# Kernel optimization log

Measured on AMD Instinct MI355X. Metric: run time of the kernel, lower is better.

Reference implementation:

```python
import jax, jax.numpy as jnp
import numpy as np

D_MODEL = 512
DK = 4
DV = 8
HIDD = 10
HEAD = D_MODEL // DV  # 64
LN_EPS = 1e-5


def setup_inputs() -> dict:
    key = jax.random.key(0)
    ks = jax.random.split(key, 10)
    B, S, Se = 8, 512, 512
    u = jax.random.uniform  # torch.rand initializer for attention weights
    n = jax.random.normal
    return {
        "x": n(ks[0], (B, S, D_MODEL), jnp.float32),
        "x_enc": n(ks[1], (B, Se, D_MODEL), jnp.float32),
        "WqM": u(ks[2], (D_MODEL, HEAD * DK), jnp.float32),
        "WkM": u(ks[3], (D_MODEL, HEAD * DK), jnp.float32),
        "WvM": u(ks[4], (D_MODEL, HEAD * DV), jnp.float32),
        "ln_g": jnp.ones((D_MODEL,), jnp.float32),
        "ln_b": jnp.zeros((D_MODEL,), jnp.float32),
        "fc1_w": n(ks[5], (HIDD, D_MODEL), jnp.float32) * (1.0 / np.sqrt(D_MODEL)),
        "fc1_b": jnp.zeros((HIDD,), jnp.float32),
        "fc2_w": n(ks[6], (D_MODEL, HIDD), jnp.float32) * (1.0 / np.sqrt(HIDD)),
        "fc2_b": jnp.zeros((D_MODEL,), jnp.float32),
    }


def _attention(Xq, Xkv, WqM, WkM, WvM, causal_mul_mask):
    # NOTE: cross-attention in the source also uses WqM/WkM/WvM (Wq/Wk/Wv unused).
    B, Sq, _ = Xq.shape
    Sk = Xkv.shape[1]
    Q = (Xq @ WqM).reshape(B, Sq, HEAD, DK)
    K = (Xkv @ WkM).reshape(B, Sk, HEAD, DK)
    V = (Xkv @ WvM).reshape(B, Sk, HEAD, DV)
    score = jnp.einsum('bqhd,bkhd->bhqk', Q, K) / np.sqrt(DK).astype(np.float32)
    if causal_mul_mask:
        # Faithful quirk: multiplicative tril mask on scores (NOT additive -inf).
        score = score * jnp.tril(jnp.ones((Sq, Sk), score.dtype))
    w = jax.nn.softmax(score, axis=-1)
    out = jnp.einsum('bhqk,bkhd->bqhd', w, V)
    return out.reshape(B, Sq, HEAD * DV)  # HEAD*DV == d_model


def _layernorm(x, g, b):
    mu = jnp.mean(x, axis=-1, keepdims=True)
    var = jnp.mean(jnp.square(x - mu), axis=-1, keepdims=True)
    return (x - mu) * jax.lax.rsqrt(var + LN_EPS) * g + b


def reference(x, x_enc, WqM, WkM, WvM, ln_g, ln_b, fc1_w, fc1_b, fc2_w, fc2_b):
    fx = _attention(x, x, WqM, WkM, WvM, causal_mul_mask=True)
    fx = _attention(fx, x_enc, WqM, WkM, WvM, causal_mul_mask=False)
    y = _layernorm(x + fx, ln_g, ln_b)
    h = jax.nn.relu(y @ fc1_w.T + fc1_b)
    return h @ fc2_w.T + fc2_b
```

## Files before the change

### kernel.cpp

```cpp
#include <hip/hip_runtime.h>
#include <math.h>

#define D_MODEL 512
#define BATCH 8
#define SEQ 512
#define HEAD 64
#define DK 4
#define DV 8
#define HIDD 10

#define MR 64
#define KC 32
#define NC 256

template <int SPLIT>
__global__ __launch_bounds__(256) void proj_kernel(
    const float* __restrict__ xq, const float* __restrict__ xkv,
    const float* __restrict__ Wq, const float* __restrict__ Wk,
    const float* __restrict__ Wv,
    float* __restrict__ Qa, float* __restrict__ Ka, float* __restrict__ Va,
    float* __restrict__ Qb, float* __restrict__ Kb, float* __restrict__ Vb)
{
    __shared__ float xt[KC * MR];
    __shared__ float wt[KC * NC];

    const int t   = threadIdx.x;
    const int bid = blockIdx.x;
    const int ks  = SPLIT ? (bid & 1) : 0;
    const int bj  = SPLIT ? ((bid >> 1) & 3) : (bid & 3);
    const int br  = SPLIT ? (bid >> 3) : (bid >> 2);
    const int r0  = br * MR;
    const int kbase = ks * 256;
    const int kend  = kbase + (SPLIT ? 256 : 512);

    const float* X; const float* W; int ldw; int c0;
    if (bj == 0)      { X = xq;  W = Wq; ldw = 256; c0 = 0;   }
    else if (bj == 1) { X = xkv; W = Wk; ldw = 256; c0 = 0;   }
    else if (bj == 2) { X = xkv; W = Wv; ldw = 512; c0 = 0;   }
    else              { X = xkv; W = Wv; ldw = 512; c0 = 256; }

    float* Q2 = ks ? Qb : Qa;
    float* K2 = ks ? Kb : Ka;
    float* V2 = ks ? Vb : Va;

    const int ct   = t & 31;
    const int rt   = t >> 5;
    const int rs   = t & 63;
    const int kx   = t >> 6;
    const int lane = t & 63;
    const int wv   = t >> 6;

    float4 accL[8], accH[8];
#pragma unroll
    for (int r = 0; r < 8; ++r) {
        accL[r] = make_float4(0.f, 0.f, 0.f, 0.f);
        accH[r] = make_float4(0.f, 0.f, 0.f, 0.f);
    }

    for (int kc = kbase; kc < kend; kc += KC) {
        {
            const float* xb = X + (long)(r0 + rs) * D_MODEL + kc + kx * 8;
            const float4 xa4 = *(const float4*)(xb);
            const float4 xb4 = *(const float4*)(xb + 4);
            xt[(kx * 8 + 0) * MR + rs] = xa4.x;
            xt[(kx * 8 + 1) * MR + rs] = xa4.y;
            xt[(kx * 8 + 2) * MR + rs] = xa4.z;
            xt[(kx * 8 + 3) * MR + rs] = xa4.w;
            xt[(kx * 8 + 4) * MR + rs] = xb4.x;
            xt[(kx * 8 + 5) * MR + rs] = xb4.y;
            xt[(kx * 8 + 6) * MR + rs] = xb4.z;
            xt[(kx * 8 + 7) * MR + rs] = xb4.w;
        }
#pragma unroll
        for (int i = 0; i < 8; ++i) {
            const int row = i * 4 + wv;
            *(float4*)(wt + row * NC + lane * 4) =
                *(const float4*)(W + (long)(kc + row) * ldw + c0 + lane * 4);
        }
        __syncthreads();

#pragma unroll 2
        for (int k = 0; k < KC; ++k) {
            const float4 w0 = *(const float4*)(wt + k * NC + ct * 4);
            const float4 w1 = *(const float4*)(wt + k * NC + 128 + ct * 4);
            const float4 x0 = *(const float4*)(xt + k * MR + rt * 8);
            const float4 x1 = *(const float4*)(xt + k * MR + rt * 8 + 4);
            const float xr[8] = {x0.x, x0.y, x0.z, x0.w, x1.x, x1.y, x1.z, x1.w};
#pragma unroll
            for (int r = 0; r < 8; ++r) {
                accL[r].x = fmaf(xr[r], w0.x, accL[r].x);
                accL[r].y = fmaf(xr[r], w0.y, accL[r].y);
                accL[r].z = fmaf(xr[r], w0.z, accL[r].z);
                accL[r].w = fmaf(xr[r], w0.w, accL[r].w);
                accH[r].x = fmaf(xr[r], w1.x, accH[r].x);
                accH[r].y = fmaf(xr[r], w1.y, accH[r].y);
                accH[r].z = fmaf(xr[r], w1.z, accH[r].z);
                accH[r].w = fmaf(xr[r], w1.w, accH[r].w);
            }
        }
        __syncthreads();
    }

    const int b  = r0 >> 9;
    const int sb = (r0 & 511) + rt * 8;
    if (bj <= 1) {
        float* dst = (bj == 0) ? Q2 : K2;
        const long hlo = ((long)b * HEAD + ct) * SEQ;
        const long hhi = ((long)b * HEAD + 32 + ct) * SEQ;
#pragma unroll
        for (int r = 0; r < 8; ++r) {
            *(float4*)(dst + (hlo + sb + r) * 4) = accL[r];
            *(float4*)(dst + (hhi + sb + r) * 4) = accH[r];
        }
    } else {
        const int clo = c0 + ct * 4;
        const int chi = clo + 128;
        const long vlo = ((long)b * HEAD + (clo >> 3)) * SEQ;
        const long vhi = ((long)b * HEAD + (chi >> 3)) * SEQ;
        const int off = (ct & 1) * 4;
#pragma unroll
        for (int r = 0; r < 8; ++r) {
            *(float4*)(V2 + (vlo + sb + r) * 8 + off) = accL[r];
            *(float4*)(V2 + (vhi + sb + r) * 8 + off) = accH[r];
        }
    }
}

template <int CAUSAL, int ADD2>
__global__ __launch_bounds__(128) void attn_kernel(
    const float* __restrict__ Qa, const float* __restrict__ Ka,
    const float* __restrict__ Va, const float* __restrict__ Qb,
    const float* __restrict__ Kb, const float* __restrict__ Vb,
    float* __restrict__ O)
{
    extern __shared__ float smem[];
    float* Kl = smem;
    float* Vl = smem + SEQ * DK;
    float* cs = Vl + SEQ * DV;

    const int t  = threadIdx.x;
    const int qh = blockIdx.x & 1;
    const int bh = blockIdx.x >> 1;
    const int b  = bh >> 6;
    const int h  = bh & 63;

    const float4* Ksa = (const float4*)(Ka + (long)bh * SEQ * DK);
    const float4* Ksb = (const float4*)(Kb + (long)bh * SEQ * DK);
#pragma unroll
    for (int i = 0; i < 4; ++i) {
        float4 v = Ksa[t + i * 128];
        if (ADD2) {
            const float4 w = Ksb[t + i * 128];
            v.x += w.x; v.y += w.y; v.z += w.z; v.w += w.w;
        }
        ((float4*)Kl)[t + i * 128] = v;
    }
    const float4* Vsa = (const float4*)(Va + (long)bh * SEQ * DV);
    const float4* Vsb = (const float4*)(Vb + (long)bh * SEQ * DV);
#pragma unroll
    for (int i = 0; i < 8; ++i) {
        float4 v = Vsa[t + i * 128];
        if (ADD2) {
            const float4 w = Vsb[t + i * 128];
            v.x += w.x; v.y += w.y; v.z += w.z; v.w += w.w;
        }
        ((float4*)Vl)[t + i * 128] = v;
    }
    __syncthreads();

    if (CAUSAL) {
#pragma unroll
        for (int w = t; w < 256; w += 128) {
            const int ch = w >> 3, d = w & 7;
            float s16 = 0.f;
#pragma unroll
            for (int i = 0; i < 16; ++i) s16 += Vl[(ch * 16 + i) * 8 + d];
            cs[ch * 8 + d] = s16;
        }
        __syncthreads();
        if (t < 8) {
            cs[256 + t] = 0.f;
            float run = 0.f;
            for (int c2 = 31; c2 >= 0; --c2) {
                run += cs[c2 * 8 + t];
                cs[c2 * 8 + t] = run;
            }
        }
        __syncthreads();
    }

    const int q0 = qh * 256 + 2 * t, q1 = q0 + 1;
    float4 qva = *(const float4*)(Qa + ((long)bh * SEQ + q0) * 4);
    float4 qvb = *(const float4*)(Qa + ((long)bh * SEQ + q1) * 4);
    if (ADD2) {
        const float4 wa = *(const float4*)(Qb + ((long)bh * SEQ + q0) * 4);
        const float4 wb = *(const float4*)(Qb + ((long)bh * SEQ + q1) * 4);
        qva.x += wa.x; qva.y += wa.y; qva.z += wa.z; qva.w += wa.w;
        qvb.x += wb.x; qvb.y += wb.y; qvb.z += wb.z; qvb.w += wb.w;
    }
    const float qa0 = qva.x*0.5f, qa1 = qva.y*0.5f, qa2 = qva.z*0.5f, qa3 = qva.w*0.5f;
    const float qb0 = qvb.x*0.5f, qb1 = qvb.y*0.5f, qb2 = qvb.z*0.5f, qb3 = qvb.w*0.5f;

    float m0 = -INFINITY, l0 = 0.f, m1 = -INFINITY, l1 = 0.f;
    float A0[8], A1[8];
#pragma unroll
    for (int d = 0; d < 8; ++d) { A0[d] = 0.f; A1[d] = 0.f; }

    const int full_end = CAUSAL ? (q0 + 1) : SEQ;

    int s0 = 0;
    for (; s0 + 8 <= full_end; s0 += 8) {
        float sa[8], sb[8];
#pragma unroll
        for (int i = 0; i < 8; ++i) {
            const float4 k4 = *(const float4*)(Kl + (s0 + i) * 4);
            sa[i] = fmaf(qa0, k4.x, fmaf(qa1, k4.y, fmaf(qa2, k4.z, qa3 * k4.w)));
            sb[i] = fmaf(qb0, k4.x, fmaf(qb1, k4.y, fmaf(qb2, k4.z, qb3 * k4.w)));
        }
        const float ga = fmaxf(fmaxf(fmaxf(sa[0], sa[1]), fmaxf(sa[2], sa[3])),
                               fmaxf(fmaxf(sa[4], sa[5]), fmaxf(sa[6], sa[7])));
        const float gb = fmaxf(fmaxf(fmaxf(sb[0], sb[1]), fmaxf(sb[2], sb[3])),
                               fmaxf(fmaxf(sb[4], sb[5]), fmaxf(sb[6], sb[7])));
        if (ga > m0) {
            const float r = __expf(m0 - ga);
            l0 *= r;
#pragma unroll
            for (int d = 0; d < 8; ++d) A0[d] *= r;
            m0 = ga;
        }
        if (gb > m1) {
            const float r = __expf(m1 - gb);
            l1 *= r;
#pragma unroll
            for (int d = 0; d < 8; ++d) A1[d] *= r;
            m1 = gb;
        }
#pragma unroll
        for (int i = 0; i < 8; ++i) {
            const float p0 = __expf(sa[i] - m0);
            const float p1 = __expf(sb[i] - m1);
            l0 += p0; l1 += p1;
            const float4 v0 = *(const float4*)(Vl + (s0 + i) * 8);
            const float4 v1 = *(const float4*)(Vl + (s0 + i) * 8 + 4);
            A0[0] = fmaf(p0, v0.x, A0[0]); A0[1] = fmaf(p0, v0.y, A0[1]);
            A0[2] = fmaf(p0, v0.z, A0[2]); A0[3] = fmaf(p0, v0.w, A0[3]);
            A0[4] = fmaf(p0, v1.x, A0[4]); A0[5] = fmaf(p0, v1.y, A0[5]);
            A0[6] = fmaf(p0, v1.z, A0[6]); A0[7] = fmaf(p0, v1.w, A0[7]);
            A1[0] = fmaf(p1, v0.x, A1[0]); A1[1] = fmaf(p1, v0.y, A1[1]);
            A1[2] = fmaf(p1, v0.z, A1[2]); A1[3] = fmaf(p1, v0.w, A1[3]);
            A1[4] = fmaf(p1, v1.x, A1[4]); A1[5] = fmaf(p1, v1.y, A1[5]);
            A1[6] = fmaf(p1, v1.z, A1[6]); A1[7] = fmaf(p1, v1.w, A1[7]);
        }
    }

    if (CAUSAL) {
        for (int s = s0; s <= q1; ++s) {
            const float4 k4 = *(const float4*)(Kl + s * 4);
            float sa = fmaf(qa0, k4.x, fmaf(qa1, k4.y, fmaf(qa2, k4.z, qa3 * k4.w)));
            float sb = fmaf(qb0, k4.x, fmaf(qb1, k4.y, fmaf(qb2, k4.z, qb3 * k4.w)));
            sa = (s <= q0) ? sa : 0.f;
            if (sa > m0) {
                const float r = __expf(m0 - sa);
                l0 *= r;
#pragma unroll
                for (int d = 0; d < 8; ++d) A0[d] *= r;
                m0 = sa;
            }
            if (sb > m1) {
                const float r = __expf(m1 - sb);
                l1 *= r;
#pragma unroll
                for (int d = 0; d < 8; ++d) A1[d] *= r;
                m1 = sb;
            }
            const float p0 = __expf(sa - m0);
            const float p1 = __expf(sb - m1);
            l0 += p0; l1 += p1;
            const float4 v0 = *(const float4*)(Vl + s * 8);
            const float4 v1 = *(const float4*)(Vl + s * 8 + 4);
            A0[0] = fmaf(p0, v0.x, A0[0]); A0[1] = fmaf(p0, v0.y, A0[1]);
            A0[2] = fmaf(p0, v0.z, A0[2]); A0[3] = fmaf(p0, v0.w, A0[3]);
            A0[4] = fmaf(p0, v1.x, A0[4]); A0[5] = fmaf(p0, v1.y, A0[5]);
            A0[6] = fmaf(p0, v1.z, A0[6]); A0[7] = fmaf(p0, v1.w, A0[7]);
            A1[0] = fmaf(p1, v0.x, A1[0]); A1[1] = fmaf(p1, v0.y, A1[1]);
            A1[2] = fmaf(p1, v0.z, A1[2]); A1[3] = fmaf(p1, v0.w, A1[3]);
            A1[4] = fmaf(p1, v1.x, A1[4]); A1[5] = fmaf(p1, v1.y, A1[5]);
            A1[6] = fmaf(p1, v1.z, A1[6]); A1[7] = fmaf(p1, v1.w, A1[7]);
        }

        const int n = SEQ - 1 - q1;
        if (n > 0) {
            const int nq  = q1 + 1;
            const int cq2 = nq >> 4;
            float sv[8];
#pragma unroll
            for (int d = 0; d < 8; ++d) sv[d] = cs[(cq2 + 1) * 8 + d];
            for (int s = nq; s < (cq2 + 1) * 16; ++s) {
                const float4 v0 = *(const float4*)(Vl + s * 8);
                const float4 v1 = *(const float4*)(Vl + s * 8 + 4);
                sv[0] += v0.x; sv[1] += v0.y; sv[2] += v0.z; sv[3] += v0.w;
                sv[4] += v1.x; sv[5] += v1.y; sv[6] += v1.z; sv[7] += v1.w;
            }
            const float pm0 = __expf(-m0);
            l0 += pm0 * (float)n;
#pragma unroll
            for (int d = 0; d < 8; ++d) A0[d] = fmaf(pm0, sv[d], A0[d]);

            const float M1  = fmaxf(m1, 0.f);
            const float r1  = __expf(m1 - M1);
            const float pm1 = __expf(-M1);
            l1 = l1 * r1 + pm1 * (float)n;
#pragma unroll
            for (int d = 0; d < 8; ++d) A1[d] = A1[d] * r1 + pm1 * sv[d];
        }
    }

    const float i0 = 1.0f / l0, i1 = 1.0f / l1;
    const long ob0 = ((long)b * SEQ + q0) * 512 + h * DV;
    const long ob1 = ((long)b * SEQ + q1) * 512 + h * DV;
    *(float4*)(O + ob0)     = make_float4(A0[0]*i0, A0[1]*i0, A0[2]*i0, A0[3]*i0);
    *(float4*)(O + ob0 + 4) = make_float4(A0[4]*i0, A0[5]*i0, A0[6]*i0, A0[7]*i0);
    *(float4*)(O + ob1)     = make_float4(A1[0]*i1, A1[1]*i1, A1[2]*i1, A1[3]*i1);
    *(float4*)(O + ob1 + 4) = make_float4(A1[4]*i1, A1[5]*i1, A1[6]*i1, A1[7]*i1);
}

__global__ __launch_bounds__(256) void ln_mlp_kernel(
    const float* __restrict__ x, const float* __restrict__ fx,
    const float* __restrict__ g, const float* __restrict__ beta,
    const float* __restrict__ w1, const float* __restrict__ b1,
    const float* __restrict__ w2, const float* __restrict__ b2,
    float* __restrict__ out)
{
    const int t = threadIdx.x;
    const int lane = t & 63;
    const int row = blockIdx.x * 4 + (t >> 6);
    const long base = (long)row * D_MODEL;
    const int e0 = lane * 8;

    const float4 xa = *(const float4*)(x + base + e0);
    const float4 xb = *(const float4*)(x + base + e0 + 4);
    const float4 fa = *(const float4*)(fx + base + e0);
    const float4 fb = *(const float4*)(fx + base + e0 + 4);
    float z[8] = {xa.x+fa.x, xa.y+fa.y, xa.z+fa.z, xa.w+fa.w,
                  xb.x+fb.x, xb.y+fb.y, xb.z+fb.z, xb.w+fb.w};

    float sum = 0.f;
#pragma unroll
    for (int j = 0; j < 8; ++j) sum += z[j];
#pragma unroll
    for (int o = 32; o > 0; o >>= 1) sum += __shfl_xor(sum, o);
    float mu = sum * (1.0f / 512.0f);

    float d[8], ss = 0.f;
#pragma unroll
    for (int j = 0; j < 8; ++j) { d[j] = z[j] - mu; ss += d[j] * d[j]; }
#pragma unroll
    for (int o = 32; o > 0; o >>= 1) ss += __shfl_xor(ss, o);
    float rs = rsqrtf(ss * (1.0f / 512.0f) + 1e-5f);

    const float4 ga = *(const float4*)(g + e0);
    const float4 gb = *(const float4*)(g + e0 + 4);
    const float4 ba = *(const float4*)(beta + e0);
    const float4 bb = *(const float4*)(beta + e0 + 4);
    const float gg[8] = {ga.x,ga.y,ga.z,ga.w,gb.x,gb.y,gb.z,gb.w};
    const float bt[8] = {ba.x,ba.y,ba.z,ba.w,bb.x,bb.y,bb.z,bb.w};
    float y[8];
#pragma unroll
    for (int j = 0; j < 8; ++j) y[j] = d[j] * rs * gg[j] + bt[j];

    float part[HIDD];
#pragma unroll
    for (int i = 0; i < HIDD; ++i) {
        const float4 wa = *(const float4*)(w1 + i * 512 + e0);
        const float4 wb = *(const float4*)(w1 + i * 512 + e0 + 4);
        part[i] = y[0]*wa.x + y[1]*wa.y + y[2]*wa.z + y[3]*wa.w
                + y[4]*wb.x + y[5]*wb.y + y[6]*wb.z + y[7]*wb.w;
    }
#pragma unroll
    for (int i = 0; i < HIDD; ++i)
#pragma unroll
        for (int o = 32; o > 0; o >>= 1) part[i] += __shfl_xor(part[i], o);

    float hv[HIDD];
#pragma unroll
    for (int i = 0; i < HIDD; ++i) hv[i] = fmaxf(part[i] + b1[i], 0.f);

    float o8[8];
#pragma unroll
    for (int j = 0; j < 8; ++j) o8[j] = b2[e0 + j];
#pragma unroll
    for (int i = 0; i < HIDD; ++i)
#pragma unroll
        for (int j = 0; j < 8; ++j)
            o8[j] = fmaf(hv[i], w2[(long)(e0 + j) * 10 + i], o8[j]);

    *(float4*)(out + base + e0)     = make_float4(o8[0], o8[1], o8[2], o8[3]);
    *(float4*)(out + base + e0 + 4) = make_float4(o8[4], o8[5], o8[6], o8[7]);
}

extern "C" void kernel_launch(void* const* d_in, const int* in_sizes, int n_in,
                              void* d_out, int out_size, void* d_ws, size_t ws_size,
                              hipStream_t stream) {
    (void)in_sizes; (void)n_in; (void)out_size;
    const float* x    = (const float*)d_in[0];
    const float* xenc = (const float*)d_in[1];
    const float* Wq   = (const float*)d_in[2];
    const float* Wk   = (const float*)d_in[3];
    const float* Wv   = (const float*)d_in[4];
    const float* ln_g = (const float*)d_in[5];
    const float* ln_b = (const float*)d_in[6];
    const float* w1   = (const float*)d_in[7];
    const float* b1   = (const float*)d_in[8];
    const float* w2   = (const float*)d_in[9];
    const float* b2   = (const float*)d_in[10];
    float* out = (float*)d_out;

    float* ws = (float*)d_ws;
    float* Qa = ws;
    float* Ka = Qa + 1048576;
    float* Va = Ka + 1048576;
    const size_t setf = 1048576 + 1048576 + 2097152;
    const bool split = ws_size >= (size_t)(2 * setf + 2097152) * 4;
    float* Qb = split ? (Va + 2097152) : Qa;
    float* Kb = split ? (Qb + 1048576) : Ka;
    float* Vb = split ? (Kb + 1048576) : Va;
    float* A  = (split ? (Vb + 2097152) : (Va + 2097152));

    const size_t lds_cross  = (size_t)(SEQ * DK + SEQ * DV) * 4;
    const size_t lds_causal = lds_cross + (size_t)(33 * DV) * 4;

    if (split) {
        proj_kernel<1><<<dim3(512), 256, 0, stream>>>(x, x, Wq, Wk, Wv,
                                                      Qa, Ka, Va, Qb, Kb, Vb);
        attn_kernel<1,1><<<dim3(BATCH * HEAD * 2), 128, lds_causal, stream>>>(
            Qa, Ka, Va, Qb, Kb, Vb, A);
        proj_kernel<1><<<dim3(512), 256, 0, stream>>>(A, xenc, Wq, Wk, Wv,
                                                      Qa, Ka, Va, Qb, Kb, Vb);
        attn_kernel<0,1><<<dim3(BATCH * HEAD * 2), 128, lds_cross, stream>>>(
            Qa, Ka, Va, Qb, Kb, Vb, A);
    } else {
        proj_kernel<0><<<dim3(256), 256, 0, stream>>>(x, x, Wq, Wk, Wv,
                                                      Qa, Ka, Va, Qb, Kb, Vb);
        attn_kernel<1,0><<<dim3(BATCH * HEAD * 2), 128, lds_causal, stream>>>(
            Qa, Ka, Va, Qb, Kb, Vb, A);
        proj_kernel<0><<<dim3(256), 256, 0, stream>>>(A, xenc, Wq, Wk, Wv,
                                                      Qa, Ka, Va, Qb, Kb, Vb);
        attn_kernel<0,0><<<dim3(BATCH * HEAD * 2), 128, lds_cross, stream>>>(
            Qa, Ka, Va, Qb, Kb, Vb, A);
    }

    ln_mlp_kernel<<<dim3(BATCH * SEQ / 4), 256, 0, stream>>>(x, A, ln_g, ln_b,
                                                             w1, b1, w2, b2, out);
}
```

Before: 349.4 us.

## Double-buffer projection GEMM tiles and merge attention query halves into one block

The projection kernel now prefetches the next K-chunk of X and W into registers while computing on the current LDS buffer, using two LDS buffers and one barrier per chunk instead of two. The aim is to hide global load latency behind the FMA loop. The attention kernel now uses 256-thread blocks covering all 512 queries of a head, so K/V are staged into LDS once per head instead of twice. The non-split fallback path is removed, which assumes the workspace is always large enough and doubles LDS use in the projection kernel.

```diff
diff --git a/kernel.cpp b/kernel.cpp
--- a/kernel.cpp
+++ b/kernel.cpp
@@ -13,7 +13,6 @@
 #define KC 32
 #define NC 256
 
-template <int SPLIT>
 __global__ __launch_bounds__(256) void proj_kernel(
     const float* __restrict__ xq, const float* __restrict__ xkv,
     const float* __restrict__ Wq, const float* __restrict__ Wk,
@@ -21,17 +20,17 @@
     float* __restrict__ Qa, float* __restrict__ Ka, float* __restrict__ Va,
     float* __restrict__ Qb, float* __restrict__ Kb, float* __restrict__ Vb)
 {
-    __shared__ float xt[KC * MR];
-    __shared__ float wt[KC * NC];
+    __shared__ float xt[2][KC * MR];
+    __shared__ float wt[2][KC * NC];
 
     const int t   = threadIdx.x;
     const int bid = blockIdx.x;
-    const int ks  = SPLIT ? (bid & 1) : 0;
-    const int bj  = SPLIT ? ((bid >> 1) & 3) : (bid & 3);
-    const int br  = SPLIT ? (bid >> 3) : (bid >> 2);
+    const int ks  = bid & 1;
+    const int bj  = (bid >> 1) & 3;
+    const int br  = bid >> 3;
     const int r0  = br * MR;
     const int kbase = ks * 256;
-    const int kend  = kbase + (SPLIT ? 256 : 512);
+    const int kend  = kbase + 256;
 
     const float* X; const float* W; int ldw; int c0;
     if (bj == 0)      { X = xq;  W = Wq; ldw = 256; c0 = 0;   }
@@ -48,7 +47,7 @@
     const int rs   = t & 63;
     const int kx   = t >> 6;
     const int lane = t & 63;
-    const int wv   = t >> 6;
+    const int wvi  = t >> 6;
 
     float4 accL[8], accH[8];
 #pragma unroll
@@ -57,34 +56,49 @@
         accH[r] = make_float4(0.f, 0.f, 0.f, 0.f);
     }
 
+    float4 px0, px1, pw[8];
+    {
+        const float* xb = X + (long)(r0 + rs) * D_MODEL + kbase + kx * 8;
+        px0 = *(const float4*)(xb);
+        px1 = *(const float4*)(xb + 4);
+#pragma unroll
+        for (int i = 0; i < 8; ++i)
+            pw[i] = *(const float4*)(W + (long)(kbase + i * 4 + wvi) * ldw + c0 + lane * 4);
+    }
+    {
+        float* xd = xt[0];
+        xd[(kx * 8 + 0) * MR + rs] = px0.x; xd[(kx * 8 + 1) * MR + rs] = px0.y;
+        xd[(kx * 8 + 2) * MR + rs] = px0.z; xd[(kx * 8 + 3) * MR + rs] = px0.w;
+        xd[(kx * 8 + 4) * MR + rs] = px1.x; xd[(kx * 8 + 5) * MR + rs] = px1.y;
+        xd[(kx * 8 + 6) * MR + rs] = px1.z; xd[(kx * 8 + 7) * MR + rs] = px1.w;
+        float* wd = wt[0];
+#pragma unroll
+        for (int i = 0; i < 8; ++i)
+            *(float4*)(wd + (i * 4 + wvi) * NC + lane * 4) = pw[i];
+    }
+    __syncthreads();
+
+    int buf = 0;
     for (int kc = kbase; kc < kend; kc += KC) {
-        {
-            const float* xb = X + (long)(r0 + rs) * D_MODEL + kc + kx * 8;
-            const float4 xa4 = *(const float4*)(xb);
-            const float4 xb4 = *(const float4*)(xb + 4);
-            xt[(kx * 8 + 0) * MR + rs] = xa4.x;
-            xt[(kx * 8 + 1) * MR + rs] = xa4.y;
-            xt[(kx * 8 + 2) * MR + rs] = xa4.z;
-            xt[(kx * 8 + 3) * MR + rs] = xa4.w;
-            xt[(kx * 8 + 4) * MR + rs] = xb4.x;
-            xt[(kx * 8 + 5) * MR + rs] = xb4.y;
-            xt[(kx * 8 + 6) * MR + rs] = xb4.z;
-            xt[(kx * 8 + 7) * MR + rs] = xb4.w;
-        }
-#pragma unroll
-        for (int i = 0; i < 8; ++i) {
-            const int row = i * 4 + wv;
-            *(float4*)(wt + row * NC + lane * 4) =
-                *(const float4*)(W + (long)(kc + row) * ldw + c0 + lane * 4);
-        }
-        __syncthreads();
-
+        const int kn = kc + KC;
+        const bool more = kn < kend;
+        if (more) {
+            const float* xb = X + (long)(r0 + rs) * D_MODEL + kn + kx * 8;
+            px0 = *(const float4*)(xb);
+            px1 = *(const float4*)(xb + 4);
+#pragma unroll
+            for (int i = 0; i < 8; ++i)
+                pw[i] = *(const float4*)(W + (long)(kn + i * 4 + wvi) * ldw + c0 + lane * 4);
+        }
+
+        const float* xs = xt[buf];
+        const float* wsrc = wt[buf];
 #pragma unroll 2
         for (int k = 0; k < KC; ++k) {
-            const float4 w0 = *(const float4*)(wt + k * NC + ct * 4);
-            const float4 w1 = *(const float4*)(wt + k * NC + 128 + ct * 4);
-            const float4 x0 = *(const float4*)(xt + k * MR + rt * 8);
-            const float4 x1 = *(const float4*)(xt + k * MR + rt * 8 + 4);
+            const float4 w0 = *(const float4*)(wsrc + k * NC + ct * 4);
+            const float4 w1 = *(const float4*)(wsrc + k * NC + 128 + ct * 4);
+            const float4 x0 = *(const float4*)(xs + k * MR + rt * 8);
+            const float4 x1 = *(const float4*)(xs + k * MR + rt * 8 + 4);
             const float xr[8] = {x0.x, x0.y, x0.z, x0.w, x1.x, x1.y, x1.z, x1.w};
 #pragma unroll
             for (int r = 0; r < 8; ++r) {
@@ -98,7 +112,21 @@
                 accH[r].w = fmaf(xr[r], w1.w, accH[r].w);
             }
         }
-        __syncthreads();
+
+        if (more) {
+            const int nb = buf ^ 1;
+            float* xd = xt[nb];
+            xd[(kx * 8 + 0) * MR + rs] = px0.x; xd[(kx * 8 + 1) * MR + rs] = px0.y;
+            xd[(kx * 8 + 2) * MR + rs] = px0.z; xd[(kx * 8 + 3) * MR + rs] = px0.w;
+            xd[(kx * 8 + 4) * MR + rs] = px1.x; xd[(kx * 8 + 5) * MR + rs] = px1.y;
+            xd[(kx * 8 + 6) * MR + rs] = px1.z; xd[(kx * 8 + 7) * MR + rs] = px1.w;
+            float* wd = wt[nb];
+#pragma unroll
+            for (int i = 0; i < 8; ++i)
+                *(float4*)(wd + (i * 4 + wvi) * NC + lane * 4) = pw[i];
+            __syncthreads();
+            buf = nb;
+        }
     }
 
     const int b  = r0 >> 9;
@@ -126,8 +154,8 @@
     }
 }
 
-template <int CAUSAL, int ADD2>
-__global__ __launch_bounds__(128) void attn_kernel(
+template <int CAUSAL>
+__global__ __launch_bounds__(256) void attn_kernel(
     const float* __restrict__ Qa, const float* __restrict__ Ka,
     const float* __restrict__ Va, const float* __restrict__ Qb,
     const float* __restrict__ Kb, const float* __restrict__ Vb,
@@ -139,44 +167,36 @@
     float* cs = Vl + SEQ * DV;
 
     const int t  = threadIdx.x;
-    const int qh = blockIdx.x & 1;
-    const int bh = blockIdx.x >> 1;
+    const int bh = blockIdx.x;
     const int b  = bh >> 6;
     const int h  = bh & 63;
 
     const float4* Ksa = (const float4*)(Ka + (long)bh * SEQ * DK);
     const float4* Ksb = (const float4*)(Kb + (long)bh * SEQ * DK);
 #pragma unroll
-    for (int i = 0; i < 4; ++i) {
-        float4 v = Ksa[t + i * 128];
-        if (ADD2) {
-            const float4 w = Ksb[t + i * 128];
-            v.x += w.x; v.y += w.y; v.z += w.z; v.w += w.w;
-        }
-        ((float4*)Kl)[t + i * 128] = v;
+    for (int i = 0; i < 2; ++i) {
+        float4 v = Ksa[t + i * 256];
+        const float4 w = Ksb[t + i * 256];
+        v.x += w.x; v.y += w.y; v.z += w.z; v.w += w.w;
+        ((float4*)Kl)[t + i * 256] = v;
     }
     const float4* Vsa = (const float4*)(Va + (long)bh * SEQ * DV);
     const float4* Vsb = (const float4*)(Vb + (long)bh * SEQ * DV);
 #pragma unroll
-    for (int i = 0; i < 8; ++i) {
-        float4 v = Vsa[t + i * 128];
-        if (ADD2) {
-            const float4 w = Vsb[t + i * 128];
-            v.x += w.x; v.y += w.y; v.z += w.z; v.w += w.w;
-        }
-        ((float4*)Vl)[t + i * 128] = v;
+    for (int i = 0; i < 4; ++i) {
+        float4 v = Vsa[t + i * 256];
+        const float4 w = Vsb[t + i * 256];
+        v.x += w.x; v.y += w.y; v.z += w.z; v.w += w.w;
+        ((float4*)Vl)[t + i * 256] = v;
     }
     __syncthreads();
 
     if (CAUSAL) {
-#pragma unroll
-        for (int w = t; w < 256; w += 128) {
-            const int ch = w >> 3, d = w & 7;
-            float s16 = 0.f;
-#pragma unroll
-            for (int i = 0; i < 16; ++i) s16 += Vl[(ch * 16 + i) * 8 + d];
-            cs[ch * 8 + d] = s16;
-        }
+        const int ch = t >> 3, d = t & 7;
+        float s16 = 0.f;
+#pragma unroll
+        for (int i = 0; i < 16; ++i) s16 += Vl[(ch * 16 + i) * 8 + d];
+        cs[ch * 8 + d] = s16;
         __syncthreads();
         if (t < 8) {
             cs[256 + t] = 0.f;
@@ -189,10 +209,10 @@
         __syncthreads();
     }
 
-    const int q0 = qh * 256 + 2 * t, q1 = q0 + 1;
+    const int q0 = 2 * t, q1 = q0 + 1;
     float4 qva = *(const float4*)(Qa + ((long)bh * SEQ + q0) * 4);
     float4 qvb = *(const float4*)(Qa + ((long)bh * SEQ + q1) * 4);
-    if (ADD2) {
+    {
         const float4 wa = *(const float4*)(Qb + ((long)bh * SEQ + q0) * 4);
         const float4 wb = *(const float4*)(Qb + ((long)bh * SEQ + q1) * 4);
         qva.x += wa.x; qva.y += wa.y; qva.z += wa.z; qva.w += wa.w;
@@ -401,7 +421,7 @@
 extern "C" void kernel_launch(void* const* d_in, const int* in_sizes, int n_in,
                               void* d_out, int out_size, void* d_ws, size_t ws_size,
                               hipStream_t stream) {
-    (void)in_sizes; (void)n_in; (void)out_size;
+    (void)in_sizes; (void)n_in; (void)out_size; (void)ws_size;
     const float* x    = (const float*)d_in[0];
     const float* xenc = (const float*)d_in[1];
     const float* Wq   = (const float*)d_in[2];
@@ -419,35 +439,23 @@
     float* Qa = ws;
     float* Ka = Qa + 1048576;
     float* Va = Ka + 1048576;
-    const size_t setf = 1048576 + 1048576 + 2097152;
-    const bool split = ws_size >= (size_t)(2 * setf + 2097152) * 4;
-    float* Qb = split ? (Va + 2097152) : Qa;
-    float* Kb = split ? (Qb + 1048576) : Ka;
-    float* Vb = split ? (Kb + 1048576) : Va;
-    float* A  = (split ? (Vb + 2097152) : (Va + 2097152));
+    float* Qb = Va + 2097152;
+    float* Kb = Qb + 1048576;
+    float* Vb = Kb + 1048576;
+    float* A  = Vb + 2097152;
 
     const size_t lds_cross  = (size_t)(SEQ * DK + SEQ * DV) * 4;
     const size_t lds_causal = lds_cross + (size_t)(33 * DV) * 4;
 
-    if (split) {
-        proj_kernel<1><<<dim3(512), 256, 0, stream>>>(x, x, Wq, Wk, Wv,
-                                                      Qa, Ka, Va, Qb, Kb, Vb);
-        attn_kernel<1,1><<<dim3(BATCH * HEAD * 2), 128, lds_causal, stream>>>(
-            Qa, Ka, Va, Qb, Kb, Vb, A);
-        proj_kernel<1><<<dim3(512), 256, 0, stream>>>(A, xenc, Wq, Wk, Wv,
-                                                      Qa, Ka, Va, Qb, Kb, Vb);
-        attn_kernel<0,1><<<dim3(BATCH * HEAD * 2), 128, lds_cross, stream>>>(
-            Qa, Ka, Va, Qb, Kb, Vb, A);
-    } else {
-        proj_kernel<0><<<dim3(256), 256, 0, stream>>>(x, x, Wq, Wk, Wv,
-                                                      Qa, Ka, Va, Qb, Kb, Vb);
-        attn_kernel<1,0><<<dim3(BATCH * HEAD * 2), 128, lds_causal, stream>>>(
-            Qa, Ka, Va, Qb, Kb, Vb, A);
-        proj_kernel<0><<<dim3(256), 256, 0, stream>>>(A, xenc, Wq, Wk, Wv,
-                                                      Qa, Ka, Va, Qb, Kb, Vb);
-        attn_kernel<0,0><<<dim3(BATCH * HEAD * 2), 128, lds_cross, stream>>>(
-            Qa, Ka, Va, Qb, Kb, Vb, A);
-    }
+    proj_kernel<<<dim3(512), 256, 0, stream>>>(x, x, Wq, Wk, Wv,
+                                               Qa, Ka, Va, Qb, Kb, Vb);
+    attn_kernel<1><<<dim3(BATCH * HEAD), 256, lds_causal, stream>>>(
+        Qa, Ka, Va, Qb, Kb, Vb, A);
+
+    proj_kernel<<<dim3(512), 256, 0, stream>>>(A, xenc, Wq, Wk, Wv,
+                                               Qa, Ka, Va, Qb, Kb, Vb);
+    attn_kernel<0><<<dim3(BATCH * HEAD), 256, lds_cross, stream>>>(
+        Qa, Ka, Va, Qb, Kb, Vb, A);
 
     ln_mlp_kernel<<<dim3(BATCH * SEQ / 4), 256, 0, stream>>>(x, A, ln_g, ln_b,
                                                              w1, b1, w2, b2, out);
```

Result: slower. 357.9 us (+2.4%).
